# Optimization experiments

Hardware: AMD Instinct MI355X
Metric: run time of the kernel (lower is better)

Reference implementation:

```python
import jax, jax.numpy as jnp
import numpy as np

LN_EPS = 1e-5


def setup_inputs() -> dict:
    key = jax.random.key(0)
    k1, k2, k3, k4 = jax.random.split(key, 4)
    b, n, d, o, m = 64, 196, 768, 196, 2
    return {
        "x": jax.random.normal(k1, (b, n, d), dtype=jnp.float32),
        "ln_w": jnp.ones((d,), dtype=jnp.float32),
        "ln_b": jnp.zeros((d,), dtype=jnp.float32),
        "sw": jax.random.normal(k2, (o, m, n), dtype=jnp.float32),
        "sb": jax.random.normal(k3, (o, m, n), dtype=jnp.float32),
        "dw": jax.random.normal(k4, (o, m), dtype=jnp.float32),
    }


def reference(x, ln_w, ln_b, sw, sb, dw):
    # LayerNorm over last dim (dim=768)
    mu = jnp.mean(x, axis=-1, keepdims=True)
    var = jnp.mean(jnp.square(x - mu), axis=-1, keepdims=True)
    y = (x - mu) * jax.lax.rsqrt(var + LN_EPS) * ln_w + ln_b  # (b, n, d)

    # Original: repeat y to (b,d,o,m,n), apply sw*y+sb, sum over n.
    # With no synapse activation / dropout this is exactly a contraction:
    # s[b,d,o,m] = sum_n sw[o,m,n]*y[b,n,d] + sum_n sb[o,m,n]
    s = jnp.einsum('bnd,omn->bdom', y, sw) + jnp.sum(sb, axis=-1)  # (b,d,o,m)

    # dendritic weighting then sum over branches m
    t = jnp.sum(dw * s, axis=-1)  # (b, d, o)

    # soma = nn.GELU (exact erf form)
    out = jax.nn.gelu(t, approximate=False)

    out = jnp.transpose(out, (0, 2, 1))  # (b, o, d) == (b, n, d)
    return x * (out + 1.0)
```

## Files before the change

### kernel.cpp

```cpp
#include <hip/hip_runtime.h>
#include <math.h>


#define B_   64
#define N_   196
#define D_   768
#define KQ   7
#define NKO  28
#define OPAD 256

typedef __attribute__((ext_vector_type(8))) short bf16x8;
typedef __attribute__((ext_vector_type(4))) float f32x4;

__device__ __forceinline__ unsigned short bf16_rne(float f) {
    unsigned u = __builtin_bit_cast(unsigned, f);
    u += 0x7FFFu + ((u >> 16) & 1u);
    return (unsigned short)(u >> 16);
}
__device__ __forceinline__ float bf16_to_f(unsigned short h) {
    unsigned u = ((unsigned)h) << 16;
    return __builtin_bit_cast(float, u);
}

__global__ void prep_w_kernel(const float* __restrict__ sw,
                              const float* __restrict__ sb,
                              const float* __restrict__ dw,
                              unsigned short* __restrict__ Wfh,
                              unsigned short* __restrict__ Wfl,
                              float* __restrict__ rowsum,
                              float* __restrict__ cvec) {
    int o = blockIdx.x;
    int t = threadIdx.x;
    float w0 = 0.f, w1 = 0.f;
    if (o < N_) { w0 = dw[o * 2 + 0]; w1 = dw[o * 2 + 1]; }
    float val = 0.f, sbp = 0.f;
    if (o < N_ && t < N_) {
        val = w0 * sw[(o * 2 + 0) * N_ + t] + w1 * sw[(o * 2 + 1) * N_ + t];
        sbp = w0 * sb[(o * 2 + 0) * N_ + t] + w1 * sb[(o * 2 + 1) * N_ + t];
    }
    if (t < KQ * 32) {
        unsigned short h = bf16_rne(val);
        int addr = (((o >> 4) * KQ + (t >> 5)) * 4 + ((t >> 3) & 3)) * 128
                 + (o & 15) * 8 + (t & 7);
        Wfh[addr] = h;
        Wfl[addr] = bf16_rne(val - bf16_to_f(h));
    }
    __shared__ float r1[256], r2[256];
    r1[t] = val; r2[t] = sbp;
    __syncthreads();
    for (int s = 128; s > 0; s >>= 1) {
        if (t < s) { r1[t] += r1[t + s]; r2[t] += r2[t + s]; }
        __syncthreads();
    }
    if (t == 0) { rowsum[o] = r1[0]; cvec[o] = r2[0]; }
}

__global__ __launch_bounds__(512) void ln_split_kernel(
    const float* __restrict__ x,
    const float* __restrict__ ln_w,
    unsigned short* __restrict__ Bh,
    unsigned short* __restrict__ Bl) {
    const int koct = blockIdx.x, b = blockIdx.y;
    const int t = threadIdx.x, w = t >> 6, lane = t & 63;
    const int k = koct * 8 + w;
    __shared__ float xs[8][768];

    float4 v0 = make_float4(0.f, 0.f, 0.f, 0.f);
    float4 v1 = v0, v2 = v0;
    if (k < N_) {
        const float4* xr = reinterpret_cast<const float4*>(x + ((size_t)b * N_ + k) * D_);
        v0 = xr[lane]; v1 = xr[lane + 64]; v2 = xr[lane + 128];
    }
    float s = v0.x + v0.y + v0.z + v0.w
            + v1.x + v1.y + v1.z + v1.w
            + v2.x + v2.y + v2.z + v2.w;
    float q = v0.x*v0.x + v0.y*v0.y + v0.z*v0.z + v0.w*v0.w
            + v1.x*v1.x + v1.y*v1.y + v1.z*v1.z + v1.w*v1.w
            + v2.x*v2.x + v2.y*v2.y + v2.z*v2.z + v2.w*v2.w;
    #pragma unroll
    for (int off = 32; off >= 1; off >>= 1) {
        s += __shfl_xor(s, off);
        q += __shfl_xor(q, off);
    }
    const float mu   = s * (1.0f / D_);
    const float var  = q * (1.0f / D_) - mu * mu;
    const float rstd = rsqrtf(var + 1e-5f);

    const float4* lw4 = reinterpret_cast<const float4*>(ln_w);
    float4 w0 = lw4[lane], w1 = lw4[lane + 64], w2 = lw4[lane + 128];
    float4 o0, o1, o2;
    o0.x = (v0.x - mu) * rstd * w0.x;  o0.y = (v0.y - mu) * rstd * w0.y;
    o0.z = (v0.z - mu) * rstd * w0.z;  o0.w = (v0.w - mu) * rstd * w0.w;
    o1.x = (v1.x - mu) * rstd * w1.x;  o1.y = (v1.y - mu) * rstd * w1.y;
    o1.z = (v1.z - mu) * rstd * w1.z;  o1.w = (v1.w - mu) * rstd * w1.w;
    o2.x = (v2.x - mu) * rstd * w2.x;  o2.y = (v2.y - mu) * rstd * w2.y;
    o2.z = (v2.z - mu) * rstd * w2.z;  o2.w = (v2.w - mu) * rstd * w2.w;
    *reinterpret_cast<float4*>(&xs[w][lane * 4])       = o0;
    *reinterpret_cast<float4*>(&xs[w][lane * 4 + 256]) = o1;
    *reinterpret_cast<float4*>(&xs[w][lane * 4 + 512]) = o2;
    __syncthreads();

    for (int d = t; d < D_; d += 512) {
        bf16x8 hv, lv;
        #pragma unroll
        for (int kk = 0; kk < 8; ++kk) {
            float v = xs[kk][d];
            unsigned short h = bf16_rne(v);
            hv[kk] = (short)h;
            lv[kk] = (short)bf16_rne(v - bf16_to_f(h));
        }
        const size_t base = (((size_t)b * NKO + koct) * D_ + d) * 8;
        *reinterpret_cast<bf16x8*>(Bh + base) = hv;
        *reinterpret_cast<bf16x8*>(Bl + base) = lv;
    }
}

__global__ __launch_bounds__(512, 4) void gemm_bpk_kernel(
    const float* __restrict__ x,
    const float* __restrict__ ln_b,
    const unsigned short* __restrict__ Wfh,
    const unsigned short* __restrict__ Wfl,
    const unsigned short* __restrict__ Bh,
    const unsigned short* __restrict__ Bl,
    const float* __restrict__ rowsum,
    const float* __restrict__ cvec,
    float* __restrict__ out) {
    const int b  = blockIdx.y;
    const int d0 = blockIdx.x * 64;
    const int t = threadIdx.x;
    const int w = t >> 6, lane = t & 63;
    const int m16 = lane & 15, g = lane >> 4;

    const float* xb = x + (size_t)b * (N_ * D_);

    f32x4 acc[2][4];
    #pragma unroll
    for (int i = 0; i < 2; ++i)
        #pragma unroll
        for (int j = 0; j < 4; ++j)
            acc[i][j] = (f32x4){0.f, 0.f, 0.f, 0.f};

    #pragma unroll
    for (int c = 0; c < KQ; ++c) {
        bf16x8 ah[2], al[2], bh[4], bl[4];
        const size_t krow = ((size_t)b * NKO + c * 4 + g) * D_;
        #pragma unroll
        for (int nf = 0; nf < 4; ++nf) {
            const size_t e = (krow + d0 + nf * 16 + m16) * 8;
            bh[nf] = *reinterpret_cast<const bf16x8*>(Bh + e);
            bl[nf] = *reinterpret_cast<const bf16x8*>(Bl + e);
        }
        #pragma unroll
        for (int mf = 0; mf < 2; ++mf) {
            const size_t ab = ((size_t)((w * 2 + mf) * KQ + c)) * 512 + lane * 8;
            ah[mf] = *reinterpret_cast<const bf16x8*>(Wfh + ab);
            al[mf] = *reinterpret_cast<const bf16x8*>(Wfl + ab);
        }
        #pragma unroll
        for (int nf = 0; nf < 4; ++nf) {
            #pragma unroll
            for (int mf = 0; mf < 2; ++mf) {
                acc[mf][nf] = __builtin_amdgcn_mfma_f32_16x16x32_bf16(ah[mf], bh[nf], acc[mf][nf], 0, 0, 0);
                acc[mf][nf] = __builtin_amdgcn_mfma_f32_16x16x32_bf16(ah[mf], bl[nf], acc[mf][nf], 0, 0, 0);
                acc[mf][nf] = __builtin_amdgcn_mfma_f32_16x16x32_bf16(al[mf], bh[nf], acc[mf][nf], 0, 0, 0);
            }
        }
    }

    float lbv[4];
    #pragma unroll
    for (int nf = 0; nf < 4; ++nf) lbv[nf] = ln_b[d0 + nf * 16 + m16];
    #pragma unroll
    for (int mf = 0; mf < 2; ++mf) {
        const int obase = (w * 2 + mf) * 16 + g * 4;
        f32x4 rs4 = *reinterpret_cast<const f32x4*>(rowsum + obase);
        f32x4 cc4 = *reinterpret_cast<const f32x4*>(cvec + obase);
        float xres[4][4];
        #pragma unroll
        for (int r = 0; r < 4; ++r) {
            const int o = obase + r;
            #pragma unroll
            for (int nf = 0; nf < 4; ++nf)
                xres[r][nf] = (o < N_) ? xb[(size_t)o * D_ + d0 + nf * 16 + m16] : 0.f;
        }
        #pragma unroll
        for (int r = 0; r < 4; ++r) {
            const int o = obase + r;
            if (o < N_) {
                #pragma unroll
                for (int nf = 0; nf < 4; ++nf) {
                    const int d = d0 + nf * 16 + m16;
                    float T = acc[mf][nf][r] + fmaf(lbv[nf], rs4[r], cc4[r]);
                    float gl = 0.5f * T * (1.0f + erff(T * 0.70710678118654752f));
                    out[((size_t)(b * N_ + o)) * D_ + d] = xres[r][nf] * (gl + 1.0f);
                }
            }
        }
    }
}

__global__ void ln_stats_kernel(const float* __restrict__ x,
                                float* __restrict__ mu,
                                float* __restrict__ rstd) {
    int wave = threadIdx.x >> 6;
    int lane = threadIdx.x & 63;
    int row  = blockIdx.x * 4 + wave;
    const float4* xr = reinterpret_cast<const float4*>(x + (size_t)row * D_);
    float4 v0 = xr[lane];
    float4 v1 = xr[lane + 64];
    float4 v2 = xr[lane + 128];
    float s = v0.x + v0.y + v0.z + v0.w
            + v1.x + v1.y + v1.z + v1.w
            + v2.x + v2.y + v2.z + v2.w;
    #pragma unroll
    for (int off = 32; off >= 1; off >>= 1) s += __shfl_xor(s, off);
    float m = s * (1.0f / D_);
    float q = 0.f;
    {
        float d;
        d = v0.x - m; q += d * d;  d = v0.y - m; q += d * d;
        d = v0.z - m; q += d * d;  d = v0.w - m; q += d * d;
        d = v1.x - m; q += d * d;  d = v1.y - m; q += d * d;
        d = v1.z - m; q += d * d;  d = v1.w - m; q += d * d;
        d = v2.x - m; q += d * d;  d = v2.y - m; q += d * d;
        d = v2.z - m; q += d * d;  d = v2.w - m; q += d * d;
    }
    #pragma unroll
    for (int off = 32; off >= 1; off >>= 1) q += __shfl_xor(q, off);
    if (lane == 0) {
        mu[row]   = m;
        rstd[row] = rsqrtf(q * (1.0f / D_) + 1e-5f);
    }
}

#define LOADC(s, c) do {                                                      \
    _Pragma("unroll")                                                         \
    for (int e = 0; e < 4; ++e) {                                             \
        const int k = (c) * 32 + w * 4 + e;                                   \
        if (k < N_) {                                                         \
            xv[s][e]  = xb[(size_t)k * D_ + d0 + lane];                       \
            mus[s][e] = mub[k];                                               \
            rss[s][e] = rsb[k];                                               \
        } else { xv[s][e] = 0.f; mus[s][e] = 0.f; rss[s][e] = 0.f; }          \
    } } while (0)

#define WRITEC(s) do {                                                        \
    short4 hv, lv; short* hp = &hv.x; short* lp = &lv.x;                      \
    _Pragma("unroll")                                                         \
    for (int e = 0; e < 4; ++e) {                                             \
        float v = (xv[s][e] - mus[s][e]) * rss[s][e];                         \
        unsigned short h = bf16_rne(v);                                       \
        hp[e] = (short)h;                                                     \
        lp[e] = (short)bf16_rne(v - bf16_to_f(h));                            \
    }                                                                         \
    const int ea = ((w >> 1) * 64 + lane) * 8 + (w & 1) * 4;                  \
    *reinterpret_cast<short4*>(&BsH[s][ea]) = hv;                             \
    *reinterpret_cast<short4*>(&BsL[s][ea]) = lv; } while (0)

#define LOADA(slot, c) do {                                                   \
    _Pragma("unroll")                                                         \
    for (int mf = 0; mf < 2; ++mf) {                                          \
        const size_t ab = ((size_t)((w * 2 + mf) * KQ + (c)) * 512) + lane * 8;\
        ah[slot][mf] = *reinterpret_cast<const bf16x8*>(Wfh + ab);            \
        al[slot][mf] = *reinterpret_cast<const bf16x8*>(Wfl + ab);            \
    } } while (0)

__global__ __launch_bounds__(512, 4) void gemm_lds_kernel(
    const float* __restrict__ x,
    const float* __restrict__ ln_w,
    const float* __restrict__ ln_b,
    const unsigned short* __restrict__ Wfh,
    const unsigned short* __restrict__ Wfl,
    const float* __restrict__ rowsum,
    const float* __restrict__ cvec,
    const float* __restrict__ mu,
    const float* __restrict__ rstd,
    float* __restrict__ out) {
    const int b  = blockIdx.y;
    const int d0 = blockIdx.x * 64;
    const int t = threadIdx.x;
    const int w = t >> 6, lane = t & 63;
    const int m16 = lane & 15, g = lane >> 4;

    __shared__ __align__(16) unsigned short BsH[2][2048];
    __shared__ __align__(16) unsigned short BsL[2][2048];

    const float* xb  = x + (size_t)b * (N_ * D_);
    const float* mub = mu + b * N_;
    const float* rsb = rstd + b * N_;

    float xv[2][4], mus[2][4], rss[2][4];
    bf16x8 ah[2][2], al[2][2];

    f32x4 acc[2][4];
    #pragma unroll
    for (int i = 0; i < 2; ++i)
        #pragma unroll
        for (int j = 0; j < 4; ++j)
            acc[i][j] = (f32x4){0.f, 0.f, 0.f, 0.f};

    LOADC(0, 0);
    LOADC(1, 1);
    LOADA(0, 0);
    WRITEC(0);
    __syncthreads();

    #pragma unroll
    for (int c = 0; c < KQ; ++c) {
        const int s = c & 1;
        if (c > 0) {
            WRITEC(s);
            __syncthreads();
        }
        if (c + 2 < KQ) LOADC(s, c + 2);
        if (c + 1 < KQ) LOADA((c + 1) & 1, c + 1);
        #pragma unroll
        for (int nf = 0; nf < 4; ++nf) {
            const int ba = (g * 64 + nf * 16 + m16) * 8;
            bf16x8 bh = *reinterpret_cast<const bf16x8*>(&BsH[s][ba]);
            bf16x8 bl = *reinterpret_cast<const bf16x8*>(&BsL[s][ba]);
            #pragma unroll
            for (int mf = 0; mf < 2; ++mf) {
                acc[mf][nf] = __builtin_amdgcn_mfma_f32_16x16x32_bf16(ah[s][mf], bh, acc[mf][nf], 0, 0, 0);
                acc[mf][nf] = __builtin_amdgcn_mfma_f32_16x16x32_bf16(ah[s][mf], bl, acc[mf][nf], 0, 0, 0);
                acc[mf][nf] = __builtin_amdgcn_mfma_f32_16x16x32_bf16(al[s][mf], bh, acc[mf][nf], 0, 0, 0);
            }
        }
    }

    float lwv[4], lbv[4];
    #pragma unroll
    for (int nf = 0; nf < 4; ++nf) {
        lwv[nf] = ln_w[d0 + nf * 16 + m16];
        lbv[nf] = ln_b[d0 + nf * 16 + m16];
    }
    #pragma unroll
    for (int mf = 0; mf < 2; ++mf) {
        #pragma unroll
        for (int r = 0; r < 4; ++r) {
            const int o = w * 32 + mf * 16 + g * 4 + r;
            if (o < N_) {
                const float rs = rowsum[o], cc = cvec[o];
                #pragma unroll
                for (int nf = 0; nf < 4; ++nf) {
                    const int d = d0 + nf * 16 + m16;
                    float T = fmaf(lwv[nf], acc[mf][nf][r], fmaf(lbv[nf], rs, cc));
                    float gl = 0.5f * T * (1.0f + erff(T * 0.70710678118654752f));
                    out[((size_t)(b * N_ + o)) * D_ + d] = xb[(size_t)o * D_ + d] * (gl + 1.0f);
                }
            }
        }
    }
}

extern "C" void kernel_launch(void* const* d_in, const int* in_sizes, int n_in,
                              void* d_out, int out_size, void* d_ws, size_t ws_size,
                              hipStream_t stream) {
    const float* x    = (const float*)d_in[0];
    const float* ln_w = (const float*)d_in[1];
    const float* ln_b = (const float*)d_in[2];
    const float* sw   = (const float*)d_in[3];
    const float* sb   = (const float*)d_in[4];
    const float* dw   = (const float*)d_in[5];
    float* out = (float*)d_out;

    float* wsf = (float*)d_ws;
    float* rowsum = wsf;
    float* cvec   = rowsum + OPAD;
    unsigned short* Wfh = (unsigned short*)(cvec + OPAD);
    unsigned short* Wfl = Wfh + OPAD * (KQ * 32);
    char* after = (char*)(Wfl + OPAD * (KQ * 32));

    const size_t bpk_elems = (size_t)B_ * NKO * D_ * 8;
    const size_t need = (size_t)(after - (char*)d_ws) + 2 * bpk_elems * sizeof(unsigned short);

    prep_w_kernel<<<OPAD, 256, 0, stream>>>(sw, sb, dw, Wfh, Wfl, rowsum, cvec);

    if (ws_size >= need) {
        unsigned short* Bh = (unsigned short*)after;
        unsigned short* Bl = Bh + bpk_elems;
        ln_split_kernel<<<dim3(NKO, B_), 512, 0, stream>>>(x, ln_w, Bh, Bl);
        gemm_bpk_kernel<<<dim3(12, B_), 512, 0, stream>>>(
            x, ln_b, Wfh, Wfl, Bh, Bl, rowsum, cvec, out);
    } else {
        float* mu   = (float*)after;
        float* rstd = mu + 12608;
        ln_stats_kernel<<<(B_ * N_) / 4, 256, 0, stream>>>(x, mu, rstd);
        gemm_lds_kernel<<<dim3(12, B_), 512, 0, stream>>>(
            x, ln_w, ln_b, Wfh, Wfl, rowsum, cvec, mu, rstd, out);
    }
}
```

Before: 55.34 us.

## Stage B tiles via global_load_lds double buffering in gemm_bpk kernel

In the precomputed-B GEMM kernel, the hi/lo bf16 B tiles are now fetched with direct global-to-LDS loads into a double-buffered shared array. Each B element is loaded once per block and shared across waves, instead of every wave reading its own copy from global memory. The A (weight) fragments are prefetched one K-step ahead in registers so loads overlap the MFMA work. The cost is a block-wide barrier each iteration and extra LDS use. It is unclear whether gemm_bpk or gemm_lds is the path that runs by default.

```diff
diff --git a/kernel.cpp b/kernel.cpp
--- a/kernel.cpp
+++ b/kernel.cpp
@@ -20,6 +20,12 @@
 __device__ __forceinline__ float bf16_to_f(unsigned short h) {
     unsigned u = ((unsigned)h) << 16;
     return __builtin_bit_cast(float, u);
+}
+
+typedef __attribute__((address_space(3))) unsigned int lds_u32_t;
+typedef const __attribute__((address_space(1))) unsigned int glb_u32_t;
+__device__ __forceinline__ void gload_lds16(const void* g, void* l) {
+    __builtin_amdgcn_global_load_lds((glb_u32_t*)g, (lds_u32_t*)l, 16, 0, 0);
 }
 
 __global__ void prep_w_kernel(const float* __restrict__ sw,
@@ -131,7 +137,16 @@
     const int w = t >> 6, lane = t & 63;
     const int m16 = lane & 15, g = lane >> 4;
 
+    __shared__ __align__(16) unsigned short BsH[2][2048];
+    __shared__ __align__(16) unsigned short BsL[2][2048];
+
     const float* xb = x + (size_t)b * (N_ * D_);
+
+    const int half = w >> 2;
+    const int cell = (w & 3) * 64 + lane;
+    const int skoct = cell >> 6, sd = cell & 63;
+    const unsigned short* sbase = (half ? Bl : Bh)
+        + (((size_t)b * NKO + skoct) * D_ + d0 + sd) * 8;
 
     f32x4 acc[2][4];
     #pragma unroll
@@ -140,31 +155,43 @@
         for (int j = 0; j < 4; ++j)
             acc[i][j] = (f32x4){0.f, 0.f, 0.f, 0.f};
 
+    bf16x8 ah[2][2], al[2][2];
+    #pragma unroll
+    for (int mf = 0; mf < 2; ++mf) {
+        const size_t ab = ((size_t)((w * 2 + mf) * KQ)) * 512 + lane * 8;
+        ah[0][mf] = *reinterpret_cast<const bf16x8*>(Wfh + ab);
+        al[0][mf] = *reinterpret_cast<const bf16x8*>(Wfl + ab);
+    }
+
+    gload_lds16(sbase, (half ? &BsL[0][cell * 8] : &BsH[0][cell * 8]));
+    __syncthreads();
+
     #pragma unroll
     for (int c = 0; c < KQ; ++c) {
-        bf16x8 ah[2], al[2], bh[4], bl[4];
-        const size_t krow = ((size_t)b * NKO + c * 4 + g) * D_;
-        #pragma unroll
-        for (int nf = 0; nf < 4; ++nf) {
-            const size_t e = (krow + d0 + nf * 16 + m16) * 8;
-            bh[nf] = *reinterpret_cast<const bf16x8*>(Bh + e);
-            bl[nf] = *reinterpret_cast<const bf16x8*>(Bl + e);
-        }
-        #pragma unroll
-        for (int mf = 0; mf < 2; ++mf) {
-            const size_t ab = ((size_t)((w * 2 + mf) * KQ + c)) * 512 + lane * 8;
-            ah[mf] = *reinterpret_cast<const bf16x8*>(Wfh + ab);
-            al[mf] = *reinterpret_cast<const bf16x8*>(Wfl + ab);
-        }
-        #pragma unroll
-        for (int nf = 0; nf < 4; ++nf) {
+        const int s = c & 1;
+        if (c + 1 < KQ) {
+            gload_lds16(sbase + (size_t)(c + 1) * 4 * D_ * 8,
+                        (half ? &BsL[s ^ 1][cell * 8] : &BsH[s ^ 1][cell * 8]));
             #pragma unroll
             for (int mf = 0; mf < 2; ++mf) {
-                acc[mf][nf] = __builtin_amdgcn_mfma_f32_16x16x32_bf16(ah[mf], bh[nf], acc[mf][nf], 0, 0, 0);
-                acc[mf][nf] = __builtin_amdgcn_mfma_f32_16x16x32_bf16(ah[mf], bl[nf], acc[mf][nf], 0, 0, 0);
-                acc[mf][nf] = __builtin_amdgcn_mfma_f32_16x16x32_bf16(al[mf], bh[nf], acc[mf][nf], 0, 0, 0);
+                const size_t ab = ((size_t)((w * 2 + mf) * KQ + c + 1)) * 512 + lane * 8;
+                ah[s ^ 1][mf] = *reinterpret_cast<const bf16x8*>(Wfh + ab);
+                al[s ^ 1][mf] = *reinterpret_cast<const bf16x8*>(Wfl + ab);
             }
         }
+        #pragma unroll
+        for (int nf = 0; nf < 4; ++nf) {
+            const int ba = (g * 64 + nf * 16 + m16) * 8;
+            bf16x8 bh = *reinterpret_cast<const bf16x8*>(&BsH[s][ba]);
+            bf16x8 bl = *reinterpret_cast<const bf16x8*>(&BsL[s][ba]);
+            #pragma unroll
+            for (int mf = 0; mf < 2; ++mf) {
+                acc[mf][nf] = __builtin_amdgcn_mfma_f32_16x16x32_bf16(ah[s][mf], bh, acc[mf][nf], 0, 0, 0);
+                acc[mf][nf] = __builtin_amdgcn_mfma_f32_16x16x32_bf16(ah[s][mf], bl, acc[mf][nf], 0, 0, 0);
+                acc[mf][nf] = __builtin_amdgcn_mfma_f32_16x16x32_bf16(al[s][mf], bh, acc[mf][nf], 0, 0, 0);
+            }
+        }
+        __syncthreads();
     }
 
     float lbv[4];
@@ -254,8 +281,8 @@
         lp[e] = (short)bf16_rne(v - bf16_to_f(h));                            \
     }                                                                         \
     const int ea = ((w >> 1) * 64 + lane) * 8 + (w & 1) * 4;                  \
-    *reinterpret_cast<short4*>(&BsH[s][ea]) = hv;                             \
-    *reinterpret_cast<short4*>(&BsL[s][ea]) = lv; } while (0)
+    *reinterpret_cast<short4*>(&FbH[s][ea]) = hv;                             \
+    *reinterpret_cast<short4*>(&FbL[s][ea]) = lv; } while (0)
 
 #define LOADA(slot, c) do {                                                   \
     _Pragma("unroll")                                                         \
@@ -282,8 +309,8 @@
     const int w = t >> 6, lane = t & 63;
     const int m16 = lane & 15, g = lane >> 4;
 
-    __shared__ __align__(16) unsigned short BsH[2][2048];
-    __shared__ __align__(16) unsigned short BsL[2][2048];
+    __shared__ __align__(16) unsigned short FbH[2][2048];
+    __shared__ __align__(16) unsigned short FbL[2][2048];
 
     const float* xb  = x + (size_t)b * (N_ * D_);
     const float* mub = mu + b * N_;
@@ -317,8 +344,8 @@
         #pragma unroll
         for (int nf = 0; nf < 4; ++nf) {
             const int ba = (g * 64 + nf * 16 + m16) * 8;
-            bf16x8 bh = *reinterpret_cast<const bf16x8*>(&BsH[s][ba]);
-            bf16x8 bl = *reinterpret_cast<const bf16x8*>(&BsL[s][ba]);
+            bf16x8 bh = *reinterpret_cast<const bf16x8*>(&FbH[s][ba]);
+            bf16x8 bl = *reinterpret_cast<const bf16x8*>(&FbL[s][ba]);
             #pragma unroll
             for (int mf = 0; mf < 2; ++mf) {
                 acc[mf][nf] = __builtin_amdgcn_mfma_f32_16x16x32_bf16(ah[s][mf], bh, acc[mf][nf], 0, 0, 0);
```

Measured after the change: 55.83 us. About the same (+0.9%).
